# Kernel optimization log

Measured on AMD Instinct MI355X. Metric: run time of the kernel, lower is better.

The kernel has to match this reference:

```python
import jax, jax.numpy as jnp
import numpy as np

B, N, D = 4, 4096, 128
LOSS_WEIGHT = 1.0  # module hardcodes self.loss_weight = 1.0


def setup_inputs() -> dict:
    key = jax.random.key(0)
    k1, k2 = jax.random.split(key)
    corr_pred = jax.random.normal(k1, (B, N, D), dtype=jnp.float32)
    corr_target = jax.random.normal(k2, (B, N, D), dtype=jnp.float32)
    return {"corr_pred": corr_pred, "corr_target": corr_target}


def chamfer_distance(x, y):
    # x: [B, N, D], y: [B, N, D]
    x2 = jnp.sum(x * x, axis=-1)                      # [B, N]  diag of x @ x^T
    y2 = jnp.sum(y * y, axis=-1)                      # [B, N]  diag of y @ y^T
    zz = jnp.einsum('bnd,bmd->bnm', x, y)             # [B, N, N]
    # P[b,i,j] = ||x_i||^2 + ||y_j||^2 - 2 x_i . y_j
    P = x2[:, :, None] + y2[:, None, :] - 2.0 * zz
    P = jnp.clip(P, 0.0, 100.0)
    return jnp.mean(jnp.min(P, axis=1)) + jnp.mean(jnp.min(P, axis=2))


def reference(corr_pred, corr_target):
    chamfer = chamfer_distance(corr_pred, corr_target)
    return LOSS_WEIGHT * chamfer / corr_target.shape[0]
```

## Files before the change

kernel.cpp:

```cpp
#include <hip/hip_runtime.h>
#include <hip/hip_bf16.h>

#define B_ 4
#define N_ 4096
#define D_ 128
#define EPB (N_ * D_)

typedef float f32x4 __attribute__((ext_vector_type(4)));
typedef int   int8v __attribute__((ext_vector_type(8)));
typedef int   int4v __attribute__((ext_vector_type(4)));

#define SQRT2 1.41421356237309515f


__global__ __launch_bounds__(256) void prep_kernel(
    const float* __restrict__ X, const float* __restrict__ Y,
    unsigned char* __restrict__ Xb, unsigned char* __restrict__ Yb,
    float* __restrict__ x2, float* __restrict__ y2)
{
    const int which = blockIdx.y;
    const float* __restrict__ src = which ? Y : X;
    unsigned char* __restrict__ dst = which ? Yb : Xb;
    float* __restrict__ nrm = which ? y2 : x2;

    const int t = threadIdx.x;
    const int r = t >> 4, c = t & 15;
    const int rgG = blockIdx.x;
    const int row = rgG * 16 + r;

    const float4 v0 = *(const float4*)(src + (size_t)row * D_ + c * 8);
    const float4 v1 = *(const float4*)(src + (size_t)row * D_ + c * 8 + 4);

    float sq = v0.x * v0.x;
    sq = fmaf(v0.y, v0.y, sq); sq = fmaf(v0.z, v0.z, sq); sq = fmaf(v0.w, v0.w, sq);
    sq = fmaf(v1.x, v1.x, sq); sq = fmaf(v1.y, v1.y, sq);
    sq = fmaf(v1.z, v1.z, sq); sq = fmaf(v1.w, v1.w, sq);
    #pragma unroll
    for (int m = 1; m < 16; m <<= 1) sq += __shfl_xor(sq, m);

    unsigned lo = 0, hi = 0;
    lo = __builtin_amdgcn_cvt_pk_fp8_f32(v0.x * SQRT2, v0.y * SQRT2, lo, false);
    lo = __builtin_amdgcn_cvt_pk_fp8_f32(v0.z * SQRT2, v0.w * SQRT2, lo, true);
    hi = __builtin_amdgcn_cvt_pk_fp8_f32(v1.x * SQRT2, v1.y * SQRT2, hi, false);
    hi = __builtin_amdgcn_cvt_pk_fp8_f32(v1.z * SQRT2, v1.w * SQRT2, hi, true);

    const int b = row >> 12;
    const int rg = (row & (N_ - 1)) >> 4;
    uint2 packed; packed.x = lo; packed.y = hi;
    *(uint2*)(dst + (size_t)b * EPB + rg * 2048 + (c >> 2) * 512
              + r * 32 + (c & 3) * 8) = packed;

    if (c == 0) nrm[row] = sq;
}


#define PREF(B0, B1, Y0, Y1, H) do {                                          \
    const int cb_ = jc * 256 + (H) * 32;                                      \
    const unsigned char* bp0_ = Yp + (size_t)(cb_ >> 4) * 2048                \
                               + quad * 512 + l16 * 32;                       \
    const int4v lo0_ = *(const int4v*)(bp0_);                                 \
    const int4v hi0_ = *(const int4v*)(bp0_ + 16);                            \
    const int4v lo1_ = *(const int4v*)(bp0_ + 2048);                          \
    const int4v hi1_ = *(const int4v*)(bp0_ + 2064);                          \
    B0 = (int8v){lo0_.x, lo0_.y, lo0_.z, lo0_.w, hi0_.x, hi0_.y, hi0_.z, hi0_.w}; \
    B1 = (int8v){lo1_.x, lo1_.y, lo1_.z, lo1_.w, hi1_.x, hi1_.y, hi1_.z, hi1_.w}; \
    Y0 = y2[(size_t)b * N_ + cb_ + l16];                                      \
    Y1 = y2[(size_t)b * N_ + cb_ + 16 + l16];                                 \
} while (0)

#define STEP(B0, B1, Y0, Y1, H) do {                                          \
    f32x4 acc0_[4], acc1_[4];                                                 \
    _Pragma("unroll")                                                         \
    for (int rt = 0; rt < 4; rt++) {                                          \
        acc0_[rt] = (f32x4){0.f, 0.f, 0.f, 0.f};                              \
        acc1_[rt] = (f32x4){0.f, 0.f, 0.f, 0.f};                              \
    }                                                                         \
    _Pragma("unroll")                                                         \
    for (int rt = 0; rt < 4; rt++) {                                          \
        acc0_[rt] = __builtin_amdgcn_mfma_scale_f32_16x16x128_f8f6f4(         \
            af[rt], B0, acc0_[rt], 0, 0, 0, 127, 0, 127);                     \
        acc1_[rt] = __builtin_amdgcn_mfma_scale_f32_16x16x128_f8f6f4(         \
            af[rt], B1, acc1_[rt], 0, 0, 0, 127, 0, 127);                     \
    }                                                                         \
    float cm0_ = 3.0e38f, cm1_ = 3.0e38f;                                     \
    _Pragma("unroll")                                                         \
    for (int rt = 0; rt < 4; rt++)                                            \
    _Pragma("unroll")                                                         \
    for (int i = 0; i < 4; i++) {                                             \
        const float xv_ = x2v[rt][i];                                         \
        const float a0_ = acc0_[rt][i], a1_ = acc1_[rt][i];                   \
        rmin[rt][i] = fminf(rmin[rt][i], fminf(Y0 - a0_, Y1 - a1_));          \
        cm0_ = fminf(cm0_, xv_ - a0_);                                        \
        cm1_ = fminf(cm1_, xv_ - a1_);                                        \
    }                                                                         \
    {                                                                         \
        const int cb_ = jc * 256 + (H) * 32;                                  \
        float v0_ = fminf(cm0_, __shfl_xor(cm0_, 16));                        \
        v0_ = fminf(v0_, __shfl_xor(v0_, 32));                                \
        float v1_ = fminf(cm1_, __shfl_xor(cm1_, 16));                        \
        v1_ = fminf(v1_, __shfl_xor(v1_, 32));                                \
        if (quad == 0) {                                                      \
            cpart[cpb + cb_ + l16] = v0_;                                     \
            cpart[cpb + cb_ + 16 + l16] = v1_;                                \
        }                                                                     \
    }                                                                         \
} while (0)

__global__ __launch_bounds__(256, 2) void chamfer_mfma(
    const unsigned char* __restrict__ Xb, const unsigned char* __restrict__ Yb,
    const float* __restrict__ x2, const float* __restrict__ y2,
    float* __restrict__ rpart, float* __restrict__ cpart)
{
    const int b = blockIdx.z;
    const int iT = blockIdx.y;
    const int jc = blockIdx.x;
    const int tid = threadIdx.x;
    const int wave = tid >> 6, lane = tid & 63;
    const int quad = lane >> 4, l16 = lane & 15;
    const int rowBase = iT * 256 + wave * 64;
    const size_t cpb = (size_t)((b * 16 + iT) * 4 + wave) * N_;
    const size_t rpb = (size_t)(b * 16 + jc) * N_;

    const unsigned char* __restrict__ Xp = Xb + (size_t)b * EPB;
    const unsigned char* __restrict__ Yp = Yb + (size_t)b * EPB;

    int8v af[4];
    #pragma unroll
    for (int rt = 0; rt < 4; rt++) {
        const unsigned char* ap = Xp + ((rowBase >> 4) + rt) * 2048
                                 + quad * 512 + l16 * 32;
        const int4v lo = *(const int4v*)(ap);
        const int4v hi = *(const int4v*)(ap + 16);
        af[rt] = (int8v){lo.x, lo.y, lo.z, lo.w, hi.x, hi.y, hi.z, hi.w};
    }
    f32x4 x2v[4];
    #pragma unroll
    for (int rt = 0; rt < 4; rt++)
        x2v[rt] = *(const f32x4*)(x2 + (size_t)b * N_ + rowBase + rt * 16 + quad * 4);

    float rmin[4][4];
    #pragma unroll
    for (int rt = 0; rt < 4; rt++)
        #pragma unroll
        for (int i = 0; i < 4; i++) rmin[rt][i] = 3.0e38f;

    int8v bA0, bA1, bB0, bB1;
    float yA0, yA1, yB0, yB1;
    PREF(bA0, bA1, yA0, yA1, 0);

    #pragma clang loop unroll(disable)
    for (int sp = 0; sp < 4; ++sp) {
        const int h0 = sp * 2;
        PREF(bB0, bB1, yB0, yB1, h0 + 1);
        STEP(bA0, bA1, yA0, yA1, h0);
        if (sp < 3)
            PREF(bA0, bA1, yA0, yA1, h0 + 2);
        STEP(bB0, bB1, yB0, yB1, h0 + 1);
    }

    #pragma unroll
    for (int rt = 0; rt < 4; rt++)
        #pragma unroll
        for (int i = 0; i < 4; i++) {
            float v = rmin[rt][i];
            #pragma unroll
            for (int m = 1; m < 16; m <<= 1) v = fminf(v, __shfl_xor(v, m));
            if (l16 == 0) {
                rpart[rpb + rowBase + rt * 16 + quad * 4 + i] =
                    fminf(fmaxf(x2v[rt][i] + v, 0.0f), 100.0f);
            }
        }
}

__global__ __launch_bounds__(256) void finalize1_kernel(
    const float* __restrict__ rpart, const float* __restrict__ cpart,
    const float* __restrict__ y2, float* __restrict__ partial)
{
    const int e_loc = threadIdx.x & 63, sg = threadIdx.x >> 6;
    const int e = blockIdx.x * 64 + e_loc;
    const int b = e >> 12, i = e & (N_ - 1);

    float rm = 3.0e38f;
    #pragma unroll
    for (int j = 0; j < 4; j++)
        rm = fminf(rm, rpart[(size_t)(b * 16 + sg * 4 + j) * N_ + i]);

    float cm = 3.0e38f;
    #pragma unroll
    for (int p = 0; p < 16; p++)
        cm = fminf(cm, cpart[(size_t)(b * 64 + sg * 16 + p) * N_ + i]);

    __shared__ float smr[4][64], smc[4][64];
    smr[sg][e_loc] = rm;
    smc[sg][e_loc] = cm;
    __syncthreads();

    if (sg == 0) {
        rm = fminf(fminf(smr[0][e_loc], smr[1][e_loc]),
                   fminf(smr[2][e_loc], smr[3][e_loc]));
        cm = fminf(fminf(smc[0][e_loc], smc[1][e_loc]),
                   fminf(smc[2][e_loc], smc[3][e_loc]));
        float s = rm + fminf(fmaxf(cm + y2[e], 0.0f), 100.0f);
        #pragma unroll
        for (int m = 1; m < 64; m <<= 1) s += __shfl_xor(s, m);
        if (e_loc == 0) partial[blockIdx.x] = s;
    }
}

__global__ __launch_bounds__(64) void finalize2_kernel(
    const float* __restrict__ partial, float* __restrict__ out)
{
    const int l = threadIdx.x;
    float s = partial[l] + partial[l + 64] + partial[l + 128] + partial[l + 192];
    #pragma unroll
    for (int m = 1; m < 64; m <<= 1) s += __shfl_xor(s, m);
    if (l == 0)
        out[0] = s / ((float)B_ * (float)N_) / (float)B_;
}

extern "C" void kernel_launch(void* const* d_in, const int* in_sizes, int n_in,
                              void* d_out, int out_size, void* d_ws, size_t ws_size,
                              hipStream_t stream) {
    const float* X = (const float*)d_in[0];
    const float* Y = (const float*)d_in[1];

    char* ws = (char*)d_ws;
    const size_t f8_bytes = (size_t)B_ * N_ * D_;
    unsigned char* Xb = (unsigned char*)ws;
    unsigned char* Yb = (unsigned char*)(ws + f8_bytes);
    char* ws2 = ws + 2 * f8_bytes;
    const size_t vec_bytes = (size_t)B_ * N_ * 4;
    float* x2      = (float*)(ws2);
    float* y2      = (float*)(ws2 + vec_bytes);
    float* rpart   = (float*)(ws2 + 2 * vec_bytes);
    float* cpart   = (float*)(ws2 + 18 * vec_bytes);
    float* partial = (float*)(ws2 + 82 * vec_bytes);
    float* out = (float*)d_out;

    prep_kernel<<<dim3(B_ * N_ / 16, 2), 256, 0, stream>>>(
        X, Y, Xb, Yb, x2, y2);
    chamfer_mfma<<<dim3(16, 16, B_), 256, 0, stream>>>(
        Xb, Yb, x2, y2, rpart, cpart);
    finalize1_kernel<<<256, 256, 0, stream>>>(rpart, cpart, y2, partial);
    finalize2_kernel<<<1, 64, 0, stream>>>(partial, out);
}
```

Measured before the change: 90.07 us.

## Drop software prefetch, skip column shuffles, raise occupancy to three blocks per SM

The main MFMA kernel loses its manual double-buffered prefetch of Y tiles in favour of a plain loop, and its launch bound moves from 2 to 3 blocks per SM, aiming for more resident waves to hide latency. The cross-quad shuffle reduction of column minima is removed: each quad now writes its own partial column minimum, which makes the cpart buffer four times larger. finalize1 is widened to 512 threads and 8 subgroups to reduce this larger cpart array. The trade-off is four times more global writes and reads of column partials, plus the loss of explicit load/compute overlap, in exchange for fewer shuffles and higher occupancy.

Result: no change. 88.69 us (-1.5%).

```diff
diff --git a/kernel.cpp b/kernel.cpp
--- a/kernel.cpp
+++ b/kernel.cpp
@@ -53,60 +53,7 @@
     if (c == 0) nrm[row] = sq;
 }
 
-
-#define PREF(B0, B1, Y0, Y1, H) do {                                          \
-    const int cb_ = jc * 256 + (H) * 32;                                      \
-    const unsigned char* bp0_ = Yp + (size_t)(cb_ >> 4) * 2048                \
-                               + quad * 512 + l16 * 32;                       \
-    const int4v lo0_ = *(const int4v*)(bp0_);                                 \
-    const int4v hi0_ = *(const int4v*)(bp0_ + 16);                            \
-    const int4v lo1_ = *(const int4v*)(bp0_ + 2048);                          \
-    const int4v hi1_ = *(const int4v*)(bp0_ + 2064);                          \
-    B0 = (int8v){lo0_.x, lo0_.y, lo0_.z, lo0_.w, hi0_.x, hi0_.y, hi0_.z, hi0_.w}; \
-    B1 = (int8v){lo1_.x, lo1_.y, lo1_.z, lo1_.w, hi1_.x, hi1_.y, hi1_.z, hi1_.w}; \
-    Y0 = y2[(size_t)b * N_ + cb_ + l16];                                      \
-    Y1 = y2[(size_t)b * N_ + cb_ + 16 + l16];                                 \
-} while (0)
-
-#define STEP(B0, B1, Y0, Y1, H) do {                                          \
-    f32x4 acc0_[4], acc1_[4];                                                 \
-    _Pragma("unroll")                                                         \
-    for (int rt = 0; rt < 4; rt++) {                                          \
-        acc0_[rt] = (f32x4){0.f, 0.f, 0.f, 0.f};                              \
-        acc1_[rt] = (f32x4){0.f, 0.f, 0.f, 0.f};                              \
-    }                                                                         \
-    _Pragma("unroll")                                                         \
-    for (int rt = 0; rt < 4; rt++) {                                          \
-        acc0_[rt] = __builtin_amdgcn_mfma_scale_f32_16x16x128_f8f6f4(         \
-            af[rt], B0, acc0_[rt], 0, 0, 0, 127, 0, 127);                     \
-        acc1_[rt] = __builtin_amdgcn_mfma_scale_f32_16x16x128_f8f6f4(         \
-            af[rt], B1, acc1_[rt], 0, 0, 0, 127, 0, 127);                     \
-    }                                                                         \
-    float cm0_ = 3.0e38f, cm1_ = 3.0e38f;                                     \
-    _Pragma("unroll")                                                         \
-    for (int rt = 0; rt < 4; rt++)                                            \
-    _Pragma("unroll")                                                         \
-    for (int i = 0; i < 4; i++) {                                             \
-        const float xv_ = x2v[rt][i];                                         \
-        const float a0_ = acc0_[rt][i], a1_ = acc1_[rt][i];                   \
-        rmin[rt][i] = fminf(rmin[rt][i], fminf(Y0 - a0_, Y1 - a1_));          \
-        cm0_ = fminf(cm0_, xv_ - a0_);                                        \
-        cm1_ = fminf(cm1_, xv_ - a1_);                                        \
-    }                                                                         \
-    {                                                                         \
-        const int cb_ = jc * 256 + (H) * 32;                                  \
-        float v0_ = fminf(cm0_, __shfl_xor(cm0_, 16));                        \
-        v0_ = fminf(v0_, __shfl_xor(v0_, 32));                                \
-        float v1_ = fminf(cm1_, __shfl_xor(cm1_, 16));                        \
-        v1_ = fminf(v1_, __shfl_xor(v1_, 32));                                \
-        if (quad == 0) {                                                      \
-            cpart[cpb + cb_ + l16] = v0_;                                     \
-            cpart[cpb + cb_ + 16 + l16] = v1_;                                \
-        }                                                                     \
-    }                                                                         \
-} while (0)
-
-__global__ __launch_bounds__(256, 2) void chamfer_mfma(
+__global__ __launch_bounds__(256, 3) void chamfer_mfma(
     const unsigned char* __restrict__ Xb, const unsigned char* __restrict__ Yb,
     const float* __restrict__ x2, const float* __restrict__ y2,
     float* __restrict__ rpart, float* __restrict__ cpart)
@@ -118,7 +65,7 @@
     const int wave = tid >> 6, lane = tid & 63;
     const int quad = lane >> 4, l16 = lane & 15;
     const int rowBase = iT * 256 + wave * 64;
-    const size_t cpb = (size_t)((b * 16 + iT) * 4 + wave) * N_;
+    const size_t cpb = (size_t)(((b * 16 + iT) * 4 + wave) * 4 + quad) * N_;
     const size_t rpb = (size_t)(b * 16 + jc) * N_;
 
     const unsigned char* __restrict__ Xp = Xb + (size_t)b * EPB;
@@ -144,18 +91,52 @@
         #pragma unroll
         for (int i = 0; i < 4; i++) rmin[rt][i] = 3.0e38f;
 
-    int8v bA0, bA1, bB0, bB1;
-    float yA0, yA1, yB0, yB1;
-    PREF(bA0, bA1, yA0, yA1, 0);
-
     #pragma clang loop unroll(disable)
-    for (int sp = 0; sp < 4; ++sp) {
-        const int h0 = sp * 2;
-        PREF(bB0, bB1, yB0, yB1, h0 + 1);
-        STEP(bA0, bA1, yA0, yA1, h0);
-        if (sp < 3)
-            PREF(bA0, bA1, yA0, yA1, h0 + 2);
-        STEP(bB0, bB1, yB0, yB1, h0 + 1);
+    for (int h = 0; h < 8; ++h) {
+        const int cb = jc * 256 + h * 32;
+        const unsigned char* bp = Yp + (size_t)(cb >> 4) * 2048
+                                 + quad * 512 + l16 * 32;
+        const int4v lo0 = *(const int4v*)(bp);
+        const int4v hi0 = *(const int4v*)(bp + 16);
+        const int4v lo1 = *(const int4v*)(bp + 2048);
+        const int4v hi1 = *(const int4v*)(bp + 2064);
+        const int8v b0 = (int8v){lo0.x, lo0.y, lo0.z, lo0.w,
+                                 hi0.x, hi0.y, hi0.z, hi0.w};
+        const int8v b1 = (int8v){lo1.x, lo1.y, lo1.z, lo1.w,
+                                 hi1.x, hi1.y, hi1.z, hi1.w};
+        const float y0 = y2[(size_t)b * N_ + cb + l16];
+        const float y1 = y2[(size_t)b * N_ + cb + 16 + l16];
+
+        f32x4 acc0[4], acc1[4];
+        #pragma unroll
+        for (int rt = 0; rt < 4; rt++) {
+            acc0[rt] = (f32x4){0.f, 0.f, 0.f, 0.f};
+            acc1[rt] = (f32x4){0.f, 0.f, 0.f, 0.f};
+        }
+        #pragma unroll
+        for (int rt = 0; rt < 4; rt++) {
+            acc0[rt] = __builtin_amdgcn_mfma_scale_f32_16x16x128_f8f6f4(
+                af[rt], b0, acc0[rt], 0, 0, 0, 127, 0, 127);
+            acc1[rt] = __builtin_amdgcn_mfma_scale_f32_16x16x128_f8f6f4(
+                af[rt], b1, acc1[rt], 0, 0, 0, 127, 0, 127);
+        }
+
+        float cm0 = 3.0e38f, cm1 = 3.0e38f;
+        #pragma unroll
+        for (int rt = 0; rt < 4; rt++) {
+            float d00 = x2v[rt][0] - acc0[rt][0], d01 = x2v[rt][1] - acc0[rt][1];
+            float d02 = x2v[rt][2] - acc0[rt][2], d03 = x2v[rt][3] - acc0[rt][3];
+            float d10 = x2v[rt][0] - acc1[rt][0], d11 = x2v[rt][1] - acc1[rt][1];
+            float d12 = x2v[rt][2] - acc1[rt][2], d13 = x2v[rt][3] - acc1[rt][3];
+            cm0 = fminf(cm0, fminf(fminf(d00, d01), fminf(d02, d03)));
+            cm1 = fminf(cm1, fminf(fminf(d10, d11), fminf(d12, d13)));
+            #pragma unroll
+            for (int i = 0; i < 4; i++)
+                rmin[rt][i] = fminf(rmin[rt][i],
+                                    fminf(y0 - acc0[rt][i], y1 - acc1[rt][i]));
+        }
+        cpart[cpb + cb + l16] = cm0;
+        cpart[cpb + cb + 16 + l16] = cm1;
     }
 
     #pragma unroll
@@ -172,7 +153,7 @@
         }
 }
 
-__global__ __launch_bounds__(256) void finalize1_kernel(
+__global__ __launch_bounds__(512) void finalize1_kernel(
     const float* __restrict__ rpart, const float* __restrict__ cpart,
     const float* __restrict__ y2, float* __restrict__ partial)
 {
@@ -182,24 +163,26 @@
 
     float rm = 3.0e38f;
     #pragma unroll
-    for (int j = 0; j < 4; j++)
-        rm = fminf(rm, rpart[(size_t)(b * 16 + sg * 4 + j) * N_ + i]);
+    for (int j = 0; j < 2; j++)
+        rm = fminf(rm, rpart[(size_t)(b * 16 + sg * 2 + j) * N_ + i]);
 
     float cm = 3.0e38f;
     #pragma unroll
-    for (int p = 0; p < 16; p++)
-        cm = fminf(cm, cpart[(size_t)(b * 64 + sg * 16 + p) * N_ + i]);
-
-    __shared__ float smr[4][64], smc[4][64];
+    for (int p = 0; p < 32; p++)
+        cm = fminf(cm, cpart[(size_t)(b * 256 + sg * 32 + p) * N_ + i]);
+
+    __shared__ float smr[8][64], smc[8][64];
     smr[sg][e_loc] = rm;
     smc[sg][e_loc] = cm;
     __syncthreads();
 
     if (sg == 0) {
-        rm = fminf(fminf(smr[0][e_loc], smr[1][e_loc]),
-                   fminf(smr[2][e_loc], smr[3][e_loc]));
-        cm = fminf(fminf(smc[0][e_loc], smc[1][e_loc]),
-                   fminf(smc[2][e_loc], smc[3][e_loc]));
+        rm = smr[0][e_loc]; cm = smc[0][e_loc];
+        #pragma unroll
+        for (int g = 1; g < 8; g++) {
+            rm = fminf(rm, smr[g][e_loc]);
+            cm = fminf(cm, smc[g][e_loc]);
+        }
         float s = rm + fminf(fmaxf(cm + y2[e], 0.0f), 100.0f);
         #pragma unroll
         for (int m = 1; m < 64; m <<= 1) s += __shfl_xor(s, m);
@@ -234,13 +217,13 @@
     float* y2      = (float*)(ws2 + vec_bytes);
     float* rpart   = (float*)(ws2 + 2 * vec_bytes);
     float* cpart   = (float*)(ws2 + 18 * vec_bytes);
-    float* partial = (float*)(ws2 + 82 * vec_bytes);
+    float* partial = (float*)(ws2 + 274 * vec_bytes);
     float* out = (float*)d_out;
 
     prep_kernel<<<dim3(B_ * N_ / 16, 2), 256, 0, stream>>>(
         X, Y, Xb, Yb, x2, y2);
     chamfer_mfma<<<dim3(16, 16, B_), 256, 0, stream>>>(
         Xb, Yb, x2, y2, rpart, cpart);
-    finalize1_kernel<<<256, 256, 0, stream>>>(rpart, cpart, y2, partial);
+    finalize1_kernel<<<256, 512, 0, stream>>>(rpart, cpart, y2, partial);
     finalize2_kernel<<<1, 64, 0, stream>>>(partial, out);
 }
```
